# Performance work log

Hardware: AMD Instinct MI355X
Metric: run time of the kernel (lower is better)

## Reference

```python
import jax, jax.numpy as jnp
import numpy as np

NUM_HEADS = 12
EPSILON = 1e-6
SCORE_SCALE = 1.0


def setup_inputs() -> dict:
    key = jax.random.key(0)
    ks = jax.random.split(key, 5)
    B, L, E = 2, 2048, 768
    x = jax.random.normal(ks[0], (B, L, E), dtype=jnp.float32)
    attention_mask = jnp.ones((B, L), dtype=jnp.int32)
    # linear params (lecun-ish scale)
    Wqkv = jax.random.normal(ks[1], (E, 3 * E), dtype=jnp.float32) / np.sqrt(E)
    bqkv = jnp.zeros((3 * E,), dtype=jnp.float32)
    Wout = jax.random.normal(ks[2], (E, E), dtype=jnp.float32) / np.sqrt(E)
    bout = jnp.zeros((E,), dtype=jnp.float32)
    return {"x": x, "attention_mask": attention_mask, "Wqkv": Wqkv,
            "bqkv": bqkv, "Wout": Wout, "bout": bout}


def reference(x, attention_mask, Wqkv, bqkv, Wout, bout):
    B, L, E = x.shape
    H = NUM_HEADS
    D = E // H
    qkv = x @ Wqkv + bqkv                      # [B,L,3E]
    q, k, v = jnp.split(qkv, 3, axis=-1)
    q = q.reshape(B, L, H, D).transpose(0, 2, 1, 3)  # [B,H,L,D]
    k = k.reshape(B, L, H, D).transpose(0, 2, 1, 3)
    v = v.reshape(B, L, H, D).transpose(0, 2, 1, 3)

    dot = jnp.einsum('bhid,bhjd->bhij', q, k)        # [B,H,L,L]
    q_sq = jnp.sum(q * q, axis=-1)[..., :, None]     # [B,H,L,1]
    k_sq = jnp.sum(k * k, axis=-1)[..., None, :]     # [B,H,1,L]
    scores = (dot * dot) / (q_sq + k_sq - 2.0 * dot + EPSILON)
    scores = scores * SCORE_SCALE

    pad = attention_mask[:, None, None, :]           # [B,1,1,L]
    scores = jnp.where(pad == 1, scores, jnp.finfo(scores.dtype).min)

    attn = jax.nn.softmax(scores, axis=-1)
    out = jnp.einsum('bhij,bhjd->bhid', attn, v)     # [B,H,L,D]
    out = out.transpose(0, 2, 1, 3).reshape(B, L, E)
    return out @ Wout + bout
```

## Files before the change

kernel.cpp:

```cpp
#include <hip/hip_runtime.h>
#include <hip/hip_bf16.h>
#include <cstdint>
#include <cstddef>


typedef __bf16 bf16_t;
typedef __bf16 bf16x8 __attribute__((ext_vector_type(8)));
typedef __bf16 bf16x4 __attribute__((ext_vector_type(4)));
typedef float floatx4 __attribute__((ext_vector_type(4)));

#define DEVI static __device__ __forceinline__

#define Bc 2
#define Lc 2048
#define Ec 768
#define Hc 12
#define Dc 64
#define N3c 2304
#define Mc 4096
#define ROWSc (Bc * Hc * Lc)

DEVI void glds16(const bf16_t* g, bf16_t* l) {
  __builtin_amdgcn_global_load_lds(
      (const __attribute__((address_space(1))) void*)g,
      (__attribute__((address_space(3))) void*)l, 16, 0, 0);
}


__global__ __launch_bounds__(256) void k_cvt(const float* __restrict__ in,
                                             bf16_t* __restrict__ out, int n) {
  int i = (blockIdx.x * 256 + threadIdx.x) * 4;
  if (i >= n) return;
  float4 v = *(const float4*)(in + i);
  bf16x4 o;
  o[0] = (bf16_t)v.x; o[1] = (bf16_t)v.y; o[2] = (bf16_t)v.z; o[3] = (bf16_t)v.w;
  *(bf16x4*)(out + i) = o;
}

__global__ __launch_bounds__(256) void k_tc(const float* __restrict__ in,
                                            bf16_t* __restrict__ out, int R, int C) {
  __shared__ float tile[32][33];
  int c0 = blockIdx.x * 32, r0 = blockIdx.y * 32;
  int tx = threadIdx.x, ty = threadIdx.y;
  #pragma unroll
  for (int i = 0; i < 32; i += 8)
    tile[ty + i][tx] = in[(size_t)(r0 + ty + i) * C + c0 + tx];
  __syncthreads();
  #pragma unroll
  for (int i = 0; i < 32; i += 8)
    out[(size_t)(c0 + ty + i) * R + r0 + tx] = (bf16_t)tile[tx][ty + i];
}


DEVI void gemm_core(const bf16_t* __restrict__ A, const bf16_t* __restrict__ Bt,
                    bf16_t* lA, bf16_t* lB, int m0, int n0, floatx4 (&acc)[4][4]) {
  const int tid = threadIdx.x, wave = tid >> 6, lane = tid & 63;
  const int wm = (wave >> 1) * 64, wn = (wave & 1) * 64;
  const int lrow = lane >> 2, lseg = lane & 3;
  const int quad = lane >> 4, r16 = lane & 15;
  for (int kk = 0; kk < 768; kk += 32) {
    glds16(A  + (size_t)(m0 + wave * 32      + lrow) * 768 + kk + lseg * 8, lA + (wave * 32) * 32);
    glds16(A  + (size_t)(m0 + wave * 32 + 16 + lrow) * 768 + kk + lseg * 8, lA + (wave * 32 + 16) * 32);
    glds16(Bt + (size_t)(n0 + wave * 32      + lrow) * 768 + kk + lseg * 8, lB + (wave * 32) * 32);
    glds16(Bt + (size_t)(n0 + wave * 32 + 16 + lrow) * 768 + kk + lseg * 8, lB + (wave * 32 + 16) * 32);
    __syncthreads();
    bf16x8 af[4], bv[4];
    #pragma unroll
    for (int mi = 0; mi < 4; mi++)
      af[mi] = *(const bf16x8*)(lA + (wm + mi * 16 + r16) * 32 + quad * 8);
    #pragma unroll
    for (int ni = 0; ni < 4; ni++)
      bv[ni] = *(const bf16x8*)(lB + (wn + ni * 16 + r16) * 32 + quad * 8);
    #pragma unroll
    for (int mi = 0; mi < 4; mi++)
      #pragma unroll
      for (int ni = 0; ni < 4; ni++)
        acc[mi][ni] = __builtin_amdgcn_mfma_f32_16x16x32_bf16(af[mi], bv[ni], acc[mi][ni], 0, 0, 0);
    __syncthreads();
  }
}

__global__ __launch_bounds__(256) void k_gemm_qkv(
    const bf16_t* __restrict__ A, const bf16_t* __restrict__ Bt,
    const float* __restrict__ bias,
    bf16_t* __restrict__ Qo, bf16_t* __restrict__ Ko, bf16_t* __restrict__ VTo) {
  __shared__ bf16_t lA[128 * 32];
  __shared__ bf16_t lB[128 * 32];
  const int m0 = blockIdx.y * 128, n0 = blockIdx.x * 128;
  const int tid = threadIdx.x, wave = tid >> 6, lane = tid & 63;
  const int wm = (wave >> 1) * 64, wn = (wave & 1) * 64;
  const int quad = lane >> 4, r16 = lane & 15;
  floatx4 acc[4][4] = {};
  gemm_core(A, Bt, lA, lB, m0, n0, acc);

  const int sec = n0 / 768;
  if (sec == 2) {
    #pragma unroll
    for (int ni = 0; ni < 4; ni++) {
      const int n = n0 + wn + ni * 16 + r16;
      const int nn = n - 1536;
      const int h = nn >> 6, d = nn & 63;
      const float bvs = bias[n];
      #pragma unroll
      for (int mi = 0; mi < 4; mi++) {
        const int m = m0 + wm + mi * 16 + quad * 4;
        const int b = m >> 11, l = m & 2047;
        bf16x4 o;
        #pragma unroll
        for (int reg = 0; reg < 4; reg++) o[reg] = (bf16_t)(acc[mi][ni][reg] + bvs);
        *(bf16x4*)(VTo + ((size_t)(b * Hc + h) * Dc + d) * Lc + l) = o;
      }
    }
  } else {
    bf16_t* dst = (sec == 0) ? Qo : Ko;
    #pragma unroll
    for (int ni = 0; ni < 4; ni++) {
      const int n = n0 + wn + ni * 16 + r16;
      const int nn = n - sec * 768;
      const int h = nn >> 6, d = nn & 63;
      const float bvs = bias[n];
      #pragma unroll
      for (int mi = 0; mi < 4; mi++) {
        #pragma unroll
        for (int reg = 0; reg < 4; reg++) {
          const int m = m0 + wm + mi * 16 + quad * 4 + reg;
          const int b = m >> 11, l = m & 2047;
          const float v = acc[mi][ni][reg] + bvs;
          dst[(((size_t)(b * Hc + h)) * Lc + l) * Dc + d] = (bf16_t)v;
        }
      }
    }
  }
}

__global__ __launch_bounds__(256) void k_gemm_out(
    const bf16_t* __restrict__ A, const bf16_t* __restrict__ Bt,
    const float* __restrict__ bias, float* __restrict__ out) {
  __shared__ bf16_t lA[128 * 32];
  __shared__ bf16_t lB[128 * 32];
  const int m0 = blockIdx.y * 128, n0 = blockIdx.x * 128;
  const int tid = threadIdx.x, wave = tid >> 6, lane = tid & 63;
  const int wm = (wave >> 1) * 64, wn = (wave & 1) * 64;
  const int quad = lane >> 4, r16 = lane & 15;
  floatx4 acc[4][4] = {};
  gemm_core(A, Bt, lA, lB, m0, n0, acc);
  #pragma unroll
  for (int ni = 0; ni < 4; ni++) {
    const int n = n0 + wn + ni * 16 + r16;
    const float bvs = bias[n];
    #pragma unroll
    for (int mi = 0; mi < 4; mi++) {
      #pragma unroll
      for (int reg = 0; reg < 4; reg++) {
        const int m = m0 + wm + mi * 16 + quad * 4 + reg;
        out[(size_t)m * Ec + n] = acc[mi][ni][reg] + bvs;
      }
    }
  }
}

__global__ __launch_bounds__(256) void k_sq(const bf16_t* __restrict__ Q,
                                            const bf16_t* __restrict__ K,
                                            const int* __restrict__ mask,
                                            float* __restrict__ qsq, float* __restrict__ ksq) {
  const int row = blockIdx.x * 256 + threadIdx.x;
  const bf16x8* q = (const bf16x8*)(Q + (size_t)row * 64);
  const bf16x8* k = (const bf16x8*)(K + (size_t)row * 64);
  float sq = 0.f, sk = 0.f;
  #pragma unroll
  for (int c = 0; c < 8; c++) {
    bf16x8 vq = q[c], vk = k[c];
    #pragma unroll
    for (int j = 0; j < 8; j++) {
      float a = (float)vq[j]; sq += a * a;
      float b = (float)vk[j]; sk += b * b;
    }
  }
  const int bh = row >> 11, l = row & 2047;
  const int b = bh / Hc;
  const int mk = mask[b * Lc + l];
  qsq[row] = sq;
  ksq[row] = (mk == 1) ? (sk + 1e-6f) : -1e30f;
}

__global__ __launch_bounds__(256) void k_attn(
    const bf16_t* __restrict__ Q, const bf16_t* __restrict__ K,
    const bf16_t* __restrict__ VT, const float* __restrict__ qsq,
    const float* __restrict__ ksq,
    float* __restrict__ Op, float* __restrict__ Mp, float* __restrict__ Lp,
    int nS) {
  __shared__ bf16_t lK[2][4096];
  __shared__ bf16_t lV[2][4096];
  __shared__ bf16_t lP[4][16 * 72];
  const int gid = blockIdx.x;
  const int s = blockIdx.y;
  const int bh = gid >> 5, qt = gid & 31;
  const int tid = threadIdx.x, wave = tid >> 6, lane = tid & 63;
  const int quad = lane >> 4, r16 = lane & 15;
  const int q0 = qt * 64 + wave * 16;
  const bf16_t* Qh = Q + ((size_t)bh * Lc) * Dc;
  const bf16_t* Kh = K + ((size_t)bh * Lc) * Dc;
  const bf16_t* VTh = VT + ((size_t)bh * Dc) * Lc;
  const float* qsqh = qsq + bh * Lc;
  const float* ksqh = ksq + bh * Lc;
  bf16_t* myP = &lP[wave][0];

  const int kt_lo = (32 * s) / nS * 64;
  const int kt_hi = (32 * (s + 1)) / nS * 64;
  const int nt = (kt_hi - kt_lo) >> 6;

  const int p0 = wave * 64 + lane;
  const int srow = p0 >> 3;
  const int sj = (p0 & 7) ^ (srow & 7);
  const bf16_t* kg0 = Kh + (size_t)(kt_lo + srow) * 64 + sj * 8;
  const bf16_t* kg1 = kg0 + 32 * 64;
  const bf16_t* vg0 = VTh + (size_t)srow * Lc + kt_lo + sj * 8;
  const bf16_t* vg1 = vg0 + 32 * Lc;
  const int ld0 = wave * 64 * 8, ld1 = (256 + wave * 64) * 8;

  const int sl0 = ((quad ^ (r16 & 7)) * 8);
  const int sl1 = sl0 ^ 32;

  bf16x8 qf0 = *(const bf16x8*)(Qh + (size_t)(q0 + r16) * 64 + quad * 8);
  bf16x8 qf1 = *(const bf16x8*)(Qh + (size_t)(q0 + r16) * 64 + 32 + quad * 8);
  const float qs = qsqh[q0 + r16];
  float mi = -1e30f, li = 0.f;
  floatx4 of[4] = {};

  glds16(kg0, &lK[0][ld0]);
  glds16(kg1, &lK[0][ld1]);
  glds16(vg0, &lV[0][ld0]);
  glds16(vg1, &lV[0][ld1]);
  kg0 += 4096; kg1 += 4096; vg0 += 64; vg1 += 64;
  __syncthreads();

  for (int t = 0; t < nt; t++) {
    const int cur = t & 1;
    if (t + 1 < nt) {
      const int nxt = cur ^ 1;
      glds16(kg0, &lK[nxt][ld0]);
      glds16(kg1, &lK[nxt][ld1]);
      glds16(vg0, &lV[nxt][ld0]);
      glds16(vg1, &lV[nxt][ld1]);
      kg0 += 4096; kg1 += 4096; vg0 += 64; vg1 += 64;
    }
    const int kt = kt_lo + t * 64;
    float4 ks4[4];
    #pragma unroll
    for (int c = 0; c < 4; c++)
      ks4[c] = *(const float4*)(ksqh + kt + c * 16 + quad * 4);
    floatx4 dot[4];
    #pragma unroll
    for (int c = 0; c < 4; c++) {
      const int rbase = (c * 16 + r16) * 64;
      bf16x8 kf0 = *(const bf16x8*)(&lK[cur][rbase + sl0]);
      bf16x8 kf1 = *(const bf16x8*)(&lK[cur][rbase + sl1]);
      floatx4 a = {};
      a = __builtin_amdgcn_mfma_f32_16x16x32_bf16(kf0, qf0, a, 0, 0, 0);
      a = __builtin_amdgcn_mfma_f32_16x16x32_bf16(kf1, qf1, a, 0, 0, 0);
      dot[c] = a;
    }
    float sv[4][4];
    float rmax = -1e30f;
    #pragma unroll
    for (int c = 0; c < 4; c++) {
      #pragma unroll
      for (int reg = 0; reg < 4; reg++) {
        const float dd = dot[c][reg];
        const float kss = ((const float*)&ks4[c])[reg];
        const float den = qs + kss - 2.f * dd;
        float sc = dd * dd * __builtin_amdgcn_rcpf(den);
        sc = (kss < 0.f) ? -1e30f : sc;
        sv[c][reg] = sc;
        rmax = fmaxf(rmax, sc);
      }
    }
    rmax = fmaxf(rmax, __shfl_xor(rmax, 16));
    rmax = fmaxf(rmax, __shfl_xor(rmax, 32));
    const float mnew = fmaxf(mi, rmax);
    const float alpha = __expf(mi - mnew);
    float psum = 0.f;
    #pragma unroll
    for (int c = 0; c < 4; c++) {
      bf16x4 pk;
      #pragma unroll
      for (int reg = 0; reg < 4; reg++) {
        const float p = __expf(sv[c][reg] - mnew);
        psum += p;
        pk[reg] = (bf16_t)p;
      }
      *(bf16x4*)(myP + r16 * 72 + c * 16 + quad * 4) = pk;
    }
    psum += __shfl_xor(psum, 16);
    psum += __shfl_xor(psum, 32);
    li = li * alpha + psum;
    mi = mnew;
    #pragma unroll
    for (int t4 = 0; t4 < 4; t4++) {
      #pragma unroll
      for (int reg = 0; reg < 4; reg++) of[t4][reg] *= alpha;
    }
    bf16x8 pf0 = *(const bf16x8*)(myP + r16 * 72 + quad * 8);
    bf16x8 pf1 = *(const bf16x8*)(myP + r16 * 72 + 32 + quad * 8);
    #pragma unroll
    for (int t4 = 0; t4 < 4; t4++) {
      const int rbase = (t4 * 16 + r16) * 64;
      bf16x8 vf0 = *(const bf16x8*)(&lV[cur][rbase + sl0]);
      bf16x8 vf1 = *(const bf16x8*)(&lV[cur][rbase + sl1]);
      of[t4] = __builtin_amdgcn_mfma_f32_16x16x32_bf16(vf0, pf0, of[t4], 0, 0, 0);
      of[t4] = __builtin_amdgcn_mfma_f32_16x16x32_bf16(vf1, pf1, of[t4], 0, 0, 0);
    }
    __syncthreads();
  }
  const size_t idx = (size_t)s * ROWSc + (size_t)bh * Lc + q0 + r16;
  #pragma unroll
  for (int t4 = 0; t4 < 4; t4++)
    *(float4*)(Op + idx * 64 + t4 * 16 + quad * 4) =
        make_float4(of[t4][0], of[t4][1], of[t4][2], of[t4][3]);
  if (lane < 16) { Mp[idx] = mi; Lp[idx] = li; }
}

__global__ __launch_bounds__(256) void k_merge(
    const float* __restrict__ Op, const float* __restrict__ Mp,
    const float* __restrict__ Lp, bf16_t* __restrict__ AO, int nS) {
  const int t = blockIdx.x * 256 + threadIdx.x;
  const int row = t >> 4, dc = (t & 15) * 4;
  float mmax = -1e30f;
  for (int s = 0; s < nS; s++) mmax = fmaxf(mmax, Mp[(size_t)s * ROWSc + row]);
  float L = 0.f;
  float o0 = 0.f, o1 = 0.f, o2 = 0.f, o3 = 0.f;
  for (int s = 0; s < nS; s++) {
    const size_t idx = (size_t)s * ROWSc + row;
    const float w = __expf(Mp[idx] - mmax);
    L += w * Lp[idx];
    const float4 v = *(const float4*)(Op + idx * 64 + dc);
    o0 += w * v.x; o1 += w * v.y; o2 += w * v.z; o3 += w * v.w;
  }
  const float inv = (L > 0.f) ? __builtin_amdgcn_rcpf(L) : 0.f;
  const int bh = row >> 11, l = row & 2047;
  const int b = bh / Hc, h = bh - b * Hc;
  bf16x4 o;
  o[0] = (bf16_t)(o0 * inv); o[1] = (bf16_t)(o1 * inv);
  o[2] = (bf16_t)(o2 * inv); o[3] = (bf16_t)(o3 * inv);
  *(bf16x4*)(AO + ((size_t)(b * Lc + l)) * Ec + h * 64 + dc) = o;
}


extern "C" void kernel_launch(void* const* d_in, const int* in_sizes, int n_in,
                              void* d_out, int out_size, void* d_ws, size_t ws_size,
                              hipStream_t stream) {
  const float* x    = (const float*)d_in[0];
  const int*   mask = (const int*)d_in[1];
  const float* Wqkv = (const float*)d_in[2];
  const float* bqkv = (const float*)d_in[3];
  const float* Wout = (const float*)d_in[4];
  const float* bout = (const float*)d_in[5];
  float* out = (float*)d_out;

  auto al = [](size_t v) { return (v + 255) & ~(size_t)255; };
  char* ws = (char*)d_ws;
  size_t off = 0;
  auto carve = [&](size_t bytes) -> char* {
    char* p = ws + off;
    off += al(bytes);
    return p;
  };
  bf16_t* WoT = (bf16_t*)carve((size_t)Ec * Ec * 2);
  bf16_t* Qb  = (bf16_t*)carve((size_t)ROWSc * Dc * 2);
  bf16_t* Kb  = (bf16_t*)carve((size_t)ROWSc * Dc * 2);
  bf16_t* VTb = (bf16_t*)carve((size_t)ROWSc * Dc * 2);
  bf16_t* AOb = (bf16_t*)carve((size_t)Mc * Ec * 2);
  float*  qsq = (float*)carve((size_t)ROWSc * 4);
  float*  ksq = (float*)carve((size_t)ROWSc * 4);
  const size_t uni = off;
  bf16_t* xb  = (bf16_t*)(ws + uni);
  bf16_t* WqT = (bf16_t*)(ws + uni + al((size_t)Mc * Ec * 2));
  const size_t ph1 = al((size_t)Mc * Ec * 2) + al((size_t)N3c * Ec * 2);
  auto ph2 = [&](int S) {
    return al((size_t)S * ROWSc * Dc * 4) + 2 * al((size_t)S * ROWSc * 4);
  };
  int S = 1;
  {
    size_t need = uni + (ph1 > ph2(2) ? ph1 : ph2(2));
    if (need <= ws_size) S = 2;
  }
  float* Op = (float*)(ws + uni);
  float* Mp = (float*)(ws + uni + al((size_t)S * ROWSc * Dc * 4));
  float* Lp = (float*)(ws + uni + al((size_t)S * ROWSc * Dc * 4) + al((size_t)S * ROWSc * 4));
  (void)in_sizes; (void)n_in; (void)out_size;

  k_cvt<<<(Mc * Ec / 4 + 255) / 256, 256, 0, stream>>>(x, xb, Mc * Ec);
  k_tc<<<dim3(N3c / 32, Ec / 32), dim3(32, 8), 0, stream>>>(Wqkv, WqT, Ec, N3c);
  k_tc<<<dim3(Ec / 32, Ec / 32), dim3(32, 8), 0, stream>>>(Wout, WoT, Ec, Ec);
  k_gemm_qkv<<<dim3(N3c / 128, Mc / 128), 256, 0, stream>>>(xb, WqT, bqkv, Qb, Kb, VTb);
  k_sq<<<ROWSc / 256, 256, 0, stream>>>(Qb, Kb, mask, qsq, ksq);
  k_attn<<<dim3(ROWSc / 64, S), 256, 0, stream>>>(Qb, Kb, VTb, qsq, ksq, Op, Mp, Lp, S);
  k_merge<<<ROWSc * 16 / 256, 256, 0, stream>>>(Op, Mp, Lp, AOb, S);
  k_gemm_out<<<dim3(Ec / 128, Mc / 128), 256, 0, stream>>>(AOb, WoT, bout, out);
}
```

Baseline: 228.4 us.

## Fuse prep kernels, single-buffer attention LDS, fp16 partials, conditional rescale, more splits

The three conversion and transpose kernels become one prep launch. The attention kernel drops LDS double buffering in favour of a single buffer with two barriers per tile, and sets a launch-bounds occupancy hint. Its online-softmax rescale is skipped when no lane's row max grows, partial outputs are stored as fp16 instead of fp32, and the KV split count rises from up to 2 to up to 4. Together these aim to cut launch count, memory traffic and VALU work and to raise occupancy, at the cost of losing load/compute overlap and some precision in the partials.

```diff
diff --git a/kernel.cpp b/kernel.cpp
--- a/kernel.cpp
+++ b/kernel.cpp
@@ -8,6 +8,8 @@
 typedef __bf16 bf16x8 __attribute__((ext_vector_type(8)));
 typedef __bf16 bf16x4 __attribute__((ext_vector_type(4)));
 typedef float floatx4 __attribute__((ext_vector_type(4)));
+typedef _Float16 half_t;
+typedef _Float16 half4 __attribute__((ext_vector_type(4)));
 
 #define DEVI static __device__ __forceinline__
 
@@ -26,22 +28,35 @@
       (__attribute__((address_space(3))) void*)l, 16, 0, 0);
 }
 
-
-__global__ __launch_bounds__(256) void k_cvt(const float* __restrict__ in,
-                                             bf16_t* __restrict__ out, int n) {
-  int i = (blockIdx.x * 256 + threadIdx.x) * 4;
-  if (i >= n) return;
-  float4 v = *(const float4*)(in + i);
-  bf16x4 o;
-  o[0] = (bf16_t)v.x; o[1] = (bf16_t)v.y; o[2] = (bf16_t)v.z; o[3] = (bf16_t)v.w;
-  *(bf16x4*)(out + i) = o;
-}
-
-__global__ __launch_bounds__(256) void k_tc(const float* __restrict__ in,
-                                            bf16_t* __restrict__ out, int R, int C) {
+#define NBCVT 3072
+#define NBTC1 1728
+#define NBTC2 576
+
+__global__ __launch_bounds__(256) void k_prep(
+    const float* __restrict__ x, bf16_t* __restrict__ xb,
+    const float* __restrict__ Wqkv, bf16_t* __restrict__ WqT,
+    const float* __restrict__ Wout, bf16_t* __restrict__ WoT) {
+  const int bid = blockIdx.x, tid = threadIdx.x;
+  if (bid < NBCVT) {
+    const int i = (bid * 256 + tid) * 4;
+    float4 v = *(const float4*)(x + i);
+    bf16x4 o;
+    o[0] = (bf16_t)v.x; o[1] = (bf16_t)v.y; o[2] = (bf16_t)v.z; o[3] = (bf16_t)v.w;
+    *(bf16x4*)(xb + i) = o;
+    return;
+  }
   __shared__ float tile[32][33];
-  int c0 = blockIdx.x * 32, r0 = blockIdx.y * 32;
-  int tx = threadIdx.x, ty = threadIdx.y;
+  const float* in; bf16_t* out; int C, bx, by;
+  if (bid < NBCVT + NBTC1) {
+    const int r = bid - NBCVT;
+    in = Wqkv; out = WqT; C = N3c; bx = r % 72; by = r / 72;
+  } else {
+    const int r = bid - NBCVT - NBTC1;
+    in = Wout; out = WoT; C = Ec; bx = r % 24; by = r / 24;
+  }
+  const int R = Ec;
+  const int c0 = bx * 32, r0 = by * 32;
+  const int tx = tid & 31, ty = tid >> 5;
   #pragma unroll
   for (int i = 0; i < 32; i += 8)
     tile[ty + i][tx] = in[(size_t)(r0 + ty + i) * C + c0 + tx];
@@ -183,14 +198,14 @@
   ksq[row] = (mk == 1) ? (sk + 1e-6f) : -1e30f;
 }
 
-__global__ __launch_bounds__(256) void k_attn(
+__global__ __launch_bounds__(256, 6) void k_attn(
     const bf16_t* __restrict__ Q, const bf16_t* __restrict__ K,
     const bf16_t* __restrict__ VT, const float* __restrict__ qsq,
     const float* __restrict__ ksq,
-    float* __restrict__ Op, float* __restrict__ Mp, float* __restrict__ Lp,
+    half_t* __restrict__ Op, float* __restrict__ Mp, float* __restrict__ Lp,
     int nS) {
-  __shared__ bf16_t lK[2][4096];
-  __shared__ bf16_t lV[2][4096];
+  __shared__ bf16_t lK[4096];
+  __shared__ bf16_t lV[4096];
   __shared__ bf16_t lP[4][16 * 72];
   const int gid = blockIdx.x;
   const int s = blockIdx.y;
@@ -227,101 +242,103 @@
   float mi = -1e30f, li = 0.f;
   floatx4 of[4] = {};
 
-  glds16(kg0, &lK[0][ld0]);
-  glds16(kg1, &lK[0][ld1]);
-  glds16(vg0, &lV[0][ld0]);
-  glds16(vg1, &lV[0][ld1]);
-  kg0 += 4096; kg1 += 4096; vg0 += 64; vg1 += 64;
-  __syncthreads();
-
   for (int t = 0; t < nt; t++) {
-    const int cur = t & 1;
-    if (t + 1 < nt) {
-      const int nxt = cur ^ 1;
-      glds16(kg0, &lK[nxt][ld0]);
-      glds16(kg1, &lK[nxt][ld1]);
-      glds16(vg0, &lV[nxt][ld0]);
-      glds16(vg1, &lV[nxt][ld1]);
-      kg0 += 4096; kg1 += 4096; vg0 += 64; vg1 += 64;
-    }
     const int kt = kt_lo + t * 64;
-    float4 ks4[4];
+    floatx4 qsk[4];
     #pragma unroll
     for (int c = 0; c < 4; c++)
-      ks4[c] = *(const float4*)(ksqh + kt + c * 16 + quad * 4);
+      qsk[c] = qs + *(const floatx4*)(ksqh + kt + c * 16 + quad * 4);
+    __syncthreads();
+    glds16(kg0, &lK[ld0]);
+    glds16(kg1, &lK[ld1]);
+    glds16(vg0, &lV[ld0]);
+    glds16(vg1, &lV[ld1]);
+    kg0 += 4096; kg1 += 4096; vg0 += 64; vg1 += 64;
+    __syncthreads();
+
     floatx4 dot[4];
     #pragma unroll
     for (int c = 0; c < 4; c++) {
       const int rbase = (c * 16 + r16) * 64;
-      bf16x8 kf0 = *(const bf16x8*)(&lK[cur][rbase + sl0]);
-      bf16x8 kf1 = *(const bf16x8*)(&lK[cur][rbase + sl1]);
+      bf16x8 kf0 = *(const bf16x8*)(&lK[rbase + sl0]);
+      bf16x8 kf1 = *(const bf16x8*)(&lK[rbase + sl1]);
       floatx4 a = {};
       a = __builtin_amdgcn_mfma_f32_16x16x32_bf16(kf0, qf0, a, 0, 0, 0);
       a = __builtin_amdgcn_mfma_f32_16x16x32_bf16(kf1, qf1, a, 0, 0, 0);
       dot[c] = a;
     }
-    float sv[4][4];
-    float rmax = -1e30f;
+    floatx4 sv4[4];
+    floatx4 mx = {-1e30f, -1e30f, -1e30f, -1e30f};
     #pragma unroll
     for (int c = 0; c < 4; c++) {
-      #pragma unroll
-      for (int reg = 0; reg < 4; reg++) {
-        const float dd = dot[c][reg];
-        const float kss = ((const float*)&ks4[c])[reg];
-        const float den = qs + kss - 2.f * dd;
-        float sc = dd * dd * __builtin_amdgcn_rcpf(den);
-        sc = (kss < 0.f) ? -1e30f : sc;
-        sv[c][reg] = sc;
-        rmax = fmaxf(rmax, sc);
-      }
-    }
+      const floatx4 den = qsk[c] - 2.f * dot[c];
+      const floatx4 num = dot[c] * dot[c];
+      floatx4 sc;
+      #pragma unroll
+      for (int e = 0; e < 4; e++) {
+        float v = num[e] * __builtin_amdgcn_rcpf(den[e]);
+        sc[e] = (qsk[c][e] < 0.f) ? -1e30f : v;
+        mx[e] = fmaxf(mx[e], sc[e]);
+      }
+      sv4[c] = sc;
+    }
+    float rmax = fmaxf(fmaxf(mx[0], mx[1]), fmaxf(mx[2], mx[3]));
     rmax = fmaxf(rmax, __shfl_xor(rmax, 16));
     rmax = fmaxf(rmax, __shfl_xor(rmax, 32));
     const float mnew = fmaxf(mi, rmax);
-    const float alpha = __expf(mi - mnew);
-    float psum = 0.f;
+    if (__ballot(rmax > mi) != 0ull) {
+      const float alpha = __expf(mi - mnew);
+      #pragma unroll
+      for (int t4 = 0; t4 < 4; t4++) {
+        #pragma unroll
+        for (int reg = 0; reg < 4; reg++) of[t4][reg] *= alpha;
+      }
+      li *= alpha;
+      mi = mnew;
+    }
+    floatx4 ps4 = {};
     #pragma unroll
     for (int c = 0; c < 4; c++) {
+      const floatx4 e4 = sv4[c] - mi;
+      floatx4 p4;
       bf16x4 pk;
       #pragma unroll
-      for (int reg = 0; reg < 4; reg++) {
-        const float p = __expf(sv[c][reg] - mnew);
-        psum += p;
-        pk[reg] = (bf16_t)p;
-      }
+      for (int e = 0; e < 4; e++) {
+        p4[e] = __expf(e4[e]);
+        pk[e] = (bf16_t)p4[e];
+      }
+      ps4 += p4;
       *(bf16x4*)(myP + r16 * 72 + c * 16 + quad * 4) = pk;
     }
+    float psum = (ps4[0] + ps4[1]) + (ps4[2] + ps4[3]);
     psum += __shfl_xor(psum, 16);
     psum += __shfl_xor(psum, 32);
-    li = li * alpha + psum;
-    mi = mnew;
-    #pragma unroll
-    for (int t4 = 0; t4 < 4; t4++) {
-      #pragma unroll
-      for (int reg = 0; reg < 4; reg++) of[t4][reg] *= alpha;
-    }
+    li += psum;
+
     bf16x8 pf0 = *(const bf16x8*)(myP + r16 * 72 + quad * 8);
     bf16x8 pf1 = *(const bf16x8*)(myP + r16 * 72 + 32 + quad * 8);
     #pragma unroll
     for (int t4 = 0; t4 < 4; t4++) {
       const int rbase = (t4 * 16 + r16) * 64;
-      bf16x8 vf0 = *(const bf16x8*)(&lV[cur][rbase + sl0]);
-      bf16x8 vf1 = *(const bf16x8*)(&lV[cur][rbase + sl1]);
+      bf16x8 vf0 = *(const bf16x8*)(&lV[rbase + sl0]);
+      bf16x8 vf1 = *(const bf16x8*)(&lV[rbase + sl1]);
       of[t4] = __builtin_amdgcn_mfma_f32_16x16x32_bf16(vf0, pf0, of[t4], 0, 0, 0);
       of[t4] = __builtin_amdgcn_mfma_f32_16x16x32_bf16(vf1, pf1, of[t4], 0, 0, 0);
     }
-    __syncthreads();
   }
   const size_t idx = (size_t)s * ROWSc + (size_t)bh * Lc + q0 + r16;
   #pragma unroll
-  for (int t4 = 0; t4 < 4; t4++)
-    *(float4*)(Op + idx * 64 + t4 * 16 + quad * 4) =
-        make_float4(of[t4][0], of[t4][1], of[t4][2], of[t4][3]);
+  for (int t4 = 0; t4 < 4; t4++) {
+    half4 o;
+    #pragma unroll
+    for (int reg = 0; reg < 4; reg++) o[reg] = (half_t)of[t4][reg];
+    *(half4*)(Op + idx * 64 + t4 * 16 + quad * 4) = o;
+  }
   if (lane < 16) { Mp[idx] = mi; Lp[idx] = li; }
 }
 
 __global__ __launch_bounds__(256) void k_merge(
-    const float* __restrict__ Op, const float* __restrict__ Mp,
+    const half_t* __restrict__ Op, const float* __restrict__ Mp,
     const float* __restrict__ Lp, bf16_t* __restrict__ AO, int nS) {
   const int t = blockIdx.x * 256 + threadIdx.x;
   const int row = t >> 4, dc = (t & 15) * 4;
@@ -333,8 +350,9 @@
     const size_t idx = (size_t)s * ROWSc + row;
     const float w = __expf(Mp[idx] - mmax);
     L += w * Lp[idx];
-    const float4 v = *(const float4*)(Op + idx * 64 + dc);
-    o0 += w * v.x; o1 += w * v.y; o2 += w * v.z; o3 += w * v.w;
+    const half4 v = *(const half4*)(Op + idx * 64 + dc);
+    o0 += w * (float)v[0]; o1 += w * (float)v[1];
+    o2 += w * (float)v[2]; o3 += w * (float)v[3];
   }
   const float inv = (L > 0.f) ? __builtin_amdgcn_rcpf(L) : 0.f;
   const int bh = row >> 11, l = row & 2047;
@@ -377,21 +395,19 @@
   bf16_t* WqT = (bf16_t*)(ws + uni + al((size_t)Mc * Ec * 2));
   const size_t ph1 = al((size_t)Mc * Ec * 2) + al((size_t)N3c * Ec * 2);
   auto ph2 = [&](int S) {
-    return al((size_t)S * ROWSc * Dc * 4) + 2 * al((size_t)S * ROWSc * 4);
+    return al((size_t)S * ROWSc * Dc * 2) + 2 * al((size_t)S * ROWSc * 4);
   };
-  int S = 1;
-  {
-    size_t need = uni + (ph1 > ph2(2) ? ph1 : ph2(2));
-    if (need <= ws_size) S = 2;
-  }
-  float* Op = (float*)(ws + uni);
-  float* Mp = (float*)(ws + uni + al((size_t)S * ROWSc * Dc * 4));
-  float* Lp = (float*)(ws + uni + al((size_t)S * ROWSc * Dc * 4) + al((size_t)S * ROWSc * 4));
+  int S = 2;
+  for (int cand : {4, 3}) {
+    size_t need = uni + (ph1 > ph2(cand) ? ph1 : ph2(cand));
+    if (need <= ws_size) { S = cand; break; }
+  }
+  half_t* Op = (half_t*)(ws + uni);
+  float*  Mp = (float*)(ws + uni + al((size_t)S * ROWSc * Dc * 2));
+  float*  Lp = (float*)(ws + uni + al((size_t)S * ROWSc * Dc * 2) + al((size_t)S * ROWSc * 4));
   (void)in_sizes; (void)n_in; (void)out_size;
 
-  k_cvt<<<(Mc * Ec / 4 + 255) / 256, 256, 0, stream>>>(x, xb, Mc * Ec);
-  k_tc<<<dim3(N3c / 32, Ec / 32), dim3(32, 8), 0, stream>>>(Wqkv, WqT, Ec, N3c);
-  k_tc<<<dim3(Ec / 32, Ec / 32), dim3(32, 8), 0, stream>>>(Wout, WoT, Ec, Ec);
+  k_prep<<<NBCVT + NBTC1 + NBTC2, 256, 0, stream>>>(x, xb, Wqkv, WqT, Wout, WoT);
   k_gemm_qkv<<<dim3(N3c / 128, Mc / 128), 256, 0, stream>>>(xb, WqT, bqkv, Qb, Kb, VTb);
   k_sq<<<ROWSc / 256, 256, 0, stream>>>(Qb, Kb, mask, qsq, ksq);
   k_attn<<<dim3(ROWSc / 64, S), 256, 0, stream>>>(Qb, Kb, VTb, qsq, ksq, Op, Mp, Lp, S);
```

Result: faster. 223.4 us (-2.2%).
